# Optimization experiments

Hardware: AMD Instinct MI355X
Metric: run time of the kernel (lower is better)

The kernel has to match this reference:

```python
import jax, jax.numpy as jnp
import numpy as np

N = 40000      # total nodes in the batched graph
E = 640000     # total edges (avg degree 16)
F_IN = 1280    # num_features (ESM embedding dim)
H = 128        # hidden_dim
G = 64         # number of graphs in the batch
OUT = 273      # output_dim (GO terms)
NEG_SLOPE = 0.2
BN_EPS = 1e-5


def setup_inputs() -> dict:
    key = jax.random.key(0)
    ks = jax.random.split(key, 16)
    def nrm(k, shape, s=0.05):
        return jax.random.normal(k, shape, dtype=jnp.float32) * s
    inp = {}
    inp["x"] = jax.random.normal(ks[0], (N, F_IN), dtype=jnp.float32)
    inp["edge_index"] = jax.random.randint(ks[1], (2, E), 0, N, dtype=jnp.int32)
    inp["batch"] = jnp.sort(jax.random.randint(ks[2], (N,), 0, G, dtype=jnp.int32))
    inp["W1"] = nrm(ks[3], (F_IN, H)); inp["b1"] = jnp.zeros((H,), jnp.float32)
    inp["a_src1"] = nrm(ks[4], (H,)); inp["a_dst1"] = nrm(ks[5], (H,))
    inp["W2"] = nrm(ks[6], (H, H)); inp["b2"] = jnp.zeros((H,), jnp.float32)
    inp["a_src2"] = nrm(ks[7], (H,)); inp["a_dst2"] = nrm(ks[8], (H,))
    inp["W3"] = nrm(ks[9], (H, H)); inp["b3"] = jnp.zeros((H,), jnp.float32)
    inp["a_src3"] = nrm(ks[10], (H,)); inp["a_dst3"] = nrm(ks[11], (H,))
    inp["fc1_W"] = nrm(ks[12], (H, 1024)); inp["fc1_b"] = jnp.zeros((1024,), jnp.float32)
    inp["bn_g"] = jnp.ones((1024,), jnp.float32); inp["bn_b"] = jnp.zeros((1024,), jnp.float32)
    inp["bn_rm"] = jnp.zeros((1024,), jnp.float32); inp["bn_rv"] = jnp.ones((1024,), jnp.float32)
    inp["fc2_W"] = nrm(ks[13], (1024, OUT)); inp["fc2_b"] = jnp.zeros((OUT,), jnp.float32)
    return inp


def gat_layer(x, W, b, a_src, a_dst, src, dst, n_nodes):
    # single-head GAT ('gat_originated'): h = xW, e_ij = lrelu(a_src.h_j + a_dst.h_i)
    h = x @ W                                            # [N, H]
    e = jax.nn.leaky_relu((h @ a_src)[src] + (h @ a_dst)[dst], NEG_SLOPE)  # [E]
    # numerically-stable segment softmax over incoming edges of each target node
    m = jax.ops.segment_max(e, dst, num_segments=n_nodes)
    p = jnp.exp(e - m[dst])
    denom = jax.ops.segment_sum(p, dst, num_segments=n_nodes)
    alpha = p / (denom[dst] + 1e-16)                     # [E]
    out = jax.ops.segment_sum(alpha[:, None] * h[src], dst, num_segments=n_nodes)
    return out + b


def reference(x, edge_index, batch, W1, b1, a_src1, a_dst1, W2, b2, a_src2, a_dst2,
              W3, b3, a_src3, a_dst3, fc1_W, fc1_b, bn_g, bn_b, bn_rm, bn_rv, fc2_W, fc2_b):
    n = x.shape[0]
    src, dst = edge_index[0], edge_index[1]
    h = jax.nn.relu(gat_layer(x, W1, b1, a_src1, a_dst1, src, dst, n))
    h = jax.nn.relu(gat_layer(h, W2, b2, a_src2, a_dst2, src, dst, n))
    h = gat_layer(h, W3, b3, a_src3, a_dst3, src, dst, n)
    # gap: global mean pool per graph
    cnt = jax.ops.segment_sum(jnp.ones((n,), h.dtype), batch, num_segments=G)
    pooled = jax.ops.segment_sum(h, batch, num_segments=G) / jnp.maximum(cnt, 1.0)[:, None]
    z = pooled @ fc1_W + fc1_b                            # [G, 1024]
    z = (z - bn_rm) * jax.lax.rsqrt(bn_rv + BN_EPS) * bn_g + bn_b  # BN eval mode
    z = jax.nn.relu(z)                                    # dropout is identity in eval
    return jax.nn.sigmoid(z @ fc2_W + fc2_b)              # [G, 273]
```

## Files before the change

### kernel.cpp

```cpp
#include <hip/hip_runtime.h>
#include <math.h>

#define N_NODES 40000
#define N_EDGES 640000
#define F_IN    1280
#define H       128
#define NG      64
#define OUTD    273
#define FC1D    1024
#define NEG_SLOPE 0.2f
#define BN_EPS  1e-5f

typedef __attribute__((ext_vector_type(8))) short short8;
typedef __attribute__((ext_vector_type(4))) float f32x4;

__device__ __forceinline__ unsigned short f2bf(float f) {
    unsigned u = __float_as_uint(f);
    u += 0x7FFF + ((u >> 16) & 1);
    return (unsigned short)(u >> 16);
}
__device__ __forceinline__ float bf2f(unsigned short s) {
    return __uint_as_float((unsigned)s << 16);
}

__global__ void edge_hist(const int* __restrict__ dst, int* __restrict__ cnt, int e) {
    int i = blockIdx.x * blockDim.x + threadIdx.x;
    if (i < e) atomicAdd(&cnt[dst[i]], 1);
}

__global__ void scan_excl(const int* __restrict__ cnt, int* __restrict__ row_ptr, int n) {
    const int CH = 40;
    __shared__ int sm[1024];
    int tid = threadIdx.x;
    int start = tid * CH;
    int local[CH];
    int s = 0;
    #pragma unroll
    for (int k = 0; k < CH; ++k) {
        int i = start + k;
        int v = (i < n) ? cnt[i] : 0;
        local[k] = s;
        s += v;
    }
    sm[tid] = s;
    __syncthreads();
    for (int off = 1; off < 1024; off <<= 1) {
        int t = (tid >= off) ? sm[tid - off] : 0;
        __syncthreads();
        sm[tid] += t;
        __syncthreads();
    }
    int base = sm[tid] - s;
    #pragma unroll
    for (int k = 0; k < CH; ++k) {
        int i = start + k;
        if (i < n) row_ptr[i] = base + local[k];
    }
    if (tid == 1023) row_ptr[n] = sm[1023];
}

__global__ void edge_fill(const int* __restrict__ src, const int* __restrict__ dst,
                          const int* __restrict__ row_ptr, int* __restrict__ fill,
                          int* __restrict__ csr_src, int e) {
    int i = blockIdx.x * blockDim.x + threadIdx.x;
    if (i < e) {
        int d = dst[i];
        int pos = row_ptr[d] + atomicAdd(&fill[d], 1);
        csr_src[pos] = src[i];
    }
}

__global__ void wprep(const float* __restrict__ W, unsigned short* __restrict__ Bp, int K) {
    int i = blockIdx.x * blockDim.x + threadIdx.x;
    if (i >= K * H) return;
    int k = i >> 7, col = i & 127;
    float v = W[i];
    unsigned short hh = f2bf(v);
    unsigned short ll = f2bf(v - bf2f(hh));
    int t = k >> 6, rr = k & 63;
    int s = rr >> 5, r5 = rr & 31;
    int laneHi = r5 >> 3, j = r5 & 7;
    int lane = laneHi * 16 + (col & 15);
    int n = col >> 4;
    int U = (n * 2 + s) * 64 + lane;
    size_t idx = (size_t)t * 16384 + (size_t)U * 8 + j;
    Bp[idx] = hh;
    Bp[idx + 8192] = ll;
}

__device__ __forceinline__ void cvt8(float4 x, float4 y, short8& hi, short8& lo) {
    float f[8] = {x.x, x.y, x.z, x.w, y.x, y.y, y.z, y.w};
    #pragma unroll
    for (int j = 0; j < 8; ++j) {
        unsigned u = __float_as_uint(f[j]);
        unsigned short hh = (unsigned short)((u + 0x7FFF + ((u >> 16) & 1)) >> 16);
        hi[j] = (short)hh;
        float r = f[j] - __uint_as_float((unsigned)hh << 16);
        unsigned ur = __float_as_uint(r);
        lo[j] = (short)((ur + 0x7FFF + ((ur >> 16) & 1)) >> 16);
    }
}

__global__ __launch_bounds__(256) void gemm_fused(
    const float* __restrict__ A, const unsigned short* __restrict__ Bp,
    const float* __restrict__ a_src, const float* __restrict__ a_dst,
    unsigned short* __restrict__ hWb, float* __restrict__ hs,
    float* __restrict__ hd, int K)
{
    __shared__ __align__(16) unsigned short lds[16384];
    const int tid  = threadIdx.x;
    const int lane = tid & 63, wv = tid >> 6;
    const int fr = lane & 15, q = lane >> 4;
    const int m0 = blockIdx.x * 64;
    const int row = m0 + wv * 16 + fr;
    const int nt = K >> 6;

    const uint4* gb = (const uint4*)Bp + tid;
    uint4* lp = (uint4*)lds + tid;

    uint4 f0 = gb[0],    f1 = gb[256],  f2 = gb[512],  f3 = gb[768],
          f4 = gb[1024], f5 = gb[1280], f6 = gb[1536], f7 = gb[1792];

    f32x4 acc0 = {}, acc1 = {}, acc2 = {}, acc3 = {},
          acc4 = {}, acc5 = {}, acc6 = {}, acc7 = {};

    for (int t = 0; t < nt; ++t) {
        lp[0] = f0;    lp[256] = f1;  lp[512] = f2;  lp[768] = f3;
        lp[1024] = f4; lp[1280] = f5; lp[1536] = f6; lp[1792] = f7;
        if (t + 1 < nt) {
            const uint4* g = gb + (size_t)(t + 1) * 2048;
            f0 = g[0];    f1 = g[256];  f2 = g[512];  f3 = g[768];
            f4 = g[1024]; f5 = g[1280]; f6 = g[1536]; f7 = g[1792];
        }
        __syncthreads();

        const float* ap = A + (size_t)row * K + t * 64 + q * 8;
        float4 a0 = *(const float4*)(ap);
        float4 a1 = *(const float4*)(ap + 4);
        float4 a2 = *(const float4*)(ap + 32);
        float4 a3 = *(const float4*)(ap + 36);

        short8 ah, al;
#define MSTEP(nn, accv, ss)                                                     \
        {                                                                       \
            const short8 bh = *(const short8*)&lds[(size_t)(((nn)*2+(ss))*64 + lane)*8];          \
            const short8 bl = *(const short8*)&lds[(size_t)(((nn)*2+(ss))*64 + lane)*8 + 8192];   \
            accv = __builtin_amdgcn_mfma_f32_16x16x32_bf16(ah, bh, accv, 0, 0, 0);                \
            accv = __builtin_amdgcn_mfma_f32_16x16x32_bf16(ah, bl, accv, 0, 0, 0);                \
            accv = __builtin_amdgcn_mfma_f32_16x16x32_bf16(al, bh, accv, 0, 0, 0);                \
        }
        cvt8(a0, a1, ah, al);
        MSTEP(0, acc0, 0) MSTEP(1, acc1, 0) MSTEP(2, acc2, 0) MSTEP(3, acc3, 0)
        MSTEP(4, acc4, 0) MSTEP(5, acc5, 0) MSTEP(6, acc6, 0) MSTEP(7, acc7, 0)
        cvt8(a2, a3, ah, al);
        MSTEP(0, acc0, 1) MSTEP(1, acc1, 1) MSTEP(2, acc2, 1) MSTEP(3, acc3, 1)
        MSTEP(4, acc4, 1) MSTEP(5, acc5, 1) MSTEP(6, acc6, 1) MSTEP(7, acc7, 1)
#undef MSTEP
        __syncthreads();
    }

    const int rb = m0 + wv * 16 + q * 4;
#define EPI(nn, accv)                                                           \
    {                                                                           \
        _Pragma("unroll")                                                       \
        for (int i = 0; i < 4; ++i)                                             \
            hWb[(size_t)(rb + i) * H + (nn)*16 + fr] = f2bf(accv[i]);           \
    }
    EPI(0, acc0) EPI(1, acc1) EPI(2, acc2) EPI(3, acc3)
    EPI(4, acc4) EPI(5, acc5) EPI(6, acc6) EPI(7, acc7)
#undef EPI

    float asv[8], adv[8];
    #pragma unroll
    for (int n = 0; n < 8; ++n) {
        asv[n] = a_src[n * 16 + fr];
        adv[n] = a_dst[n * 16 + fr];
    }
    #pragma unroll
    for (int i = 0; i < 4; ++i) {
        float ss = acc0[i]*asv[0] + acc1[i]*asv[1] + acc2[i]*asv[2] + acc3[i]*asv[3]
                 + acc4[i]*asv[4] + acc5[i]*asv[5] + acc6[i]*asv[6] + acc7[i]*asv[7];
        float dd = acc0[i]*adv[0] + acc1[i]*adv[1] + acc2[i]*adv[2] + acc3[i]*adv[3]
                 + acc4[i]*adv[4] + acc5[i]*adv[5] + acc6[i]*adv[6] + acc7[i]*adv[7];
        #pragma unroll
        for (int off = 8; off; off >>= 1) {
            ss += __shfl_xor(ss, off);
            dd += __shfl_xor(dd, off);
        }
        if (fr == 0) { hs[rb + i] = ss; hd[rb + i] = dd; }
    }
}

__device__ __forceinline__ float bfhi(unsigned u) { return __uint_as_float(u << 16); }
__device__ __forceinline__ float bflo(unsigned u) { return __uint_as_float(u & 0xffff0000u); }

__global__ void attn_agg(const unsigned short* __restrict__ hWb,
                         const float* __restrict__ hs, const float* __restrict__ hd,
                         const int* __restrict__ row_ptr, const int* __restrict__ csr_src,
                         const float* __restrict__ bias, float* __restrict__ out,
                         int n, int relu_flag) {
    int wv = (blockIdx.x * blockDim.x + threadIdx.x) >> 6;
    int lane = threadIdx.x & 63;
    if (wv >= n) return;
    int p0 = row_ptr[wv], p1 = row_ptr[wv + 1];
    int deg = p1 - p0;
    float hdi = hd[wv];
    float ax = 0.f, ay = 0.f;
    const unsigned* hb = (const unsigned*)hWb;

    if (deg <= 64) {
        int valid = (lane < deg);
        int sidx = valid ? csr_src[p0 + lane] : 0;
        float e = hs[sidx] + hdi;
        e = (e >= 0.f) ? e : NEG_SLOPE * e;
        float ev = valid ? e : -3.4e38f;
        float m = ev;
        #pragma unroll
        for (int off = 32; off; off >>= 1) m = fmaxf(m, __shfl_xor(m, off));
        float pe = valid ? __expf(e - m) : 0.f;
        float dsum = pe;
        #pragma unroll
        for (int off = 32; off; off >>= 1) dsum += __shfl_xor(dsum, off);
        pe *= 1.f / (dsum + 1e-16f);

        int j = 0;
        int dq = deg & ~3;
        for (; j < dq; j += 4) {
            float al0 = __shfl(pe, j),     al1 = __shfl(pe, j + 1);
            float al2 = __shfl(pe, j + 2), al3 = __shfl(pe, j + 3);
            int s0 = __shfl(sidx, j),     s1 = __shfl(sidx, j + 1);
            int s2 = __shfl(sidx, j + 2), s3 = __shfl(sidx, j + 3);
            unsigned u0 = hb[(size_t)s0 * 64 + lane];
            unsigned u1 = hb[(size_t)s1 * 64 + lane];
            unsigned u2 = hb[(size_t)s2 * 64 + lane];
            unsigned u3 = hb[(size_t)s3 * 64 + lane];
            ax += al0 * bfhi(u0); ay += al0 * bflo(u0);
            ax += al1 * bfhi(u1); ay += al1 * bflo(u1);
            ax += al2 * bfhi(u2); ay += al2 * bflo(u2);
            ax += al3 * bfhi(u3); ay += al3 * bflo(u3);
        }
        for (; j < deg; ++j) {
            float alpha = __shfl(pe, j);
            int s = __shfl(sidx, j);
            unsigned u = hb[(size_t)s * 64 + lane];
            ax += alpha * bfhi(u); ay += alpha * bflo(u);
        }
    } else {
        float m = -3.4e38f;
        for (int p = p0 + lane; p < p1; p += 64) {
            float e = hs[csr_src[p]] + hdi;
            e = (e >= 0.f) ? e : NEG_SLOPE * e;
            m = fmaxf(m, e);
        }
        #pragma unroll
        for (int off = 32; off; off >>= 1) m = fmaxf(m, __shfl_xor(m, off));
        float dsum = 0.f;
        for (int p = p0 + lane; p < p1; p += 64) {
            float e = hs[csr_src[p]] + hdi;
            e = (e >= 0.f) ? e : NEG_SLOPE * e;
            dsum += __expf(e - m);
        }
        #pragma unroll
        for (int off = 32; off; off >>= 1) dsum += __shfl_xor(dsum, off);
        float inv = 1.f / (dsum + 1e-16f);
        for (int p = p0; p < p1; ++p) {
            int s = csr_src[p];
            float e = hs[s] + hdi;
            e = (e >= 0.f) ? e : NEG_SLOPE * e;
            float alpha = __expf(e - m) * inv;
            unsigned u = hb[(size_t)s * 64 + lane];
            ax += alpha * bfhi(u); ay += alpha * bflo(u);
        }
    }
    float2 bv = *(const float2*)&bias[2 * lane];
    float o0 = ax + bv.x;
    float o1 = ay + bv.y;
    if (relu_flag) { o0 = fmaxf(o0, 0.f); o1 = fmaxf(o1, 0.f); }
    float2 ov; ov.x = o0; ov.y = o1;
    *(float2*)&out[(size_t)wv * H + 2 * lane] = ov;
}

__device__ __forceinline__ void graph_range(const int* __restrict__ batch, int n,
                                            int g, int& start, int& end) {
    int lo = 0, hi = n;
    while (lo < hi) { int mid = (lo + hi) >> 1; if (batch[mid] < g) lo = mid + 1; else hi = mid; }
    start = lo;
    lo = start; hi = n;
    while (lo < hi) { int mid = (lo + hi) >> 1; if (batch[mid] < g + 1) lo = mid + 1; else hi = mid; }
    end = lo;
}

__global__ void pool_part(const float* __restrict__ h, const int* __restrict__ batch,
                          float* __restrict__ part, int n) {
    int g = blockIdx.x >> 3, c = blockIdx.x & 7;
    int f = threadIdx.x;
    int start, end;
    graph_range(batch, n, g, start, end);
    int len = end - start;
    int cs = start + (len * c) / 8, ce = start + (len * (c + 1)) / 8;
    float acc = 0.f;
    for (int i = cs; i < ce; ++i) acc += h[(size_t)i * H + f];
    part[((size_t)g * 8 + c) * H + f] = acc;
}

__global__ void pool_final(const float* __restrict__ part, const int* __restrict__ batch,
                           float* __restrict__ pooled, int n) {
    int g = blockIdx.x;
    int f = threadIdx.x;
    int start, end;
    graph_range(batch, n, g, start, end);
    float s = 0.f;
    #pragma unroll
    for (int c = 0; c < 8; ++c) s += part[((size_t)g * 8 + c) * H + f];
    float cnt = (float)(end - start);
    pooled[g * H + f] = s / fmaxf(cnt, 1.f);
}

__global__ void fc1_bn_relu(const float* __restrict__ pooled, const float* __restrict__ W,
                            const float* __restrict__ b, const float* __restrict__ bng,
                            const float* __restrict__ bnb, const float* __restrict__ bnrm,
                            const float* __restrict__ bnrv, float* __restrict__ z) {
    int g = blockIdx.x >> 2;
    int j = ((blockIdx.x & 3) << 8) + threadIdx.x;
    const float* pr = pooled + g * H;
    float acc = b[j];
    #pragma unroll 8
    for (int k = 0; k < H; ++k) acc += pr[k] * W[k * FC1D + j];
    float v = (acc - bnrm[j]) * rsqrtf(bnrv[j] + BN_EPS) * bng[j] + bnb[j];
    z[g * FC1D + j] = fmaxf(v, 0.f);
}

__global__ void fc2_sig(const float* __restrict__ z, const float* __restrict__ W,
                        const float* __restrict__ b, float* __restrict__ out) {
    int g = blockIdx.x;
    int j = threadIdx.x;
    if (j >= OUTD) return;
    const float* zr = z + g * FC1D;
    float acc = b[j];
    #pragma unroll 4
    for (int k = 0; k < FC1D; ++k) acc += zr[k] * W[k * OUTD + j];
    out[g * OUTD + j] = 1.f / (1.f + __expf(-acc));
}

extern "C" void kernel_launch(void* const* d_in, const int* in_sizes, int n_in,
                              void* d_out, int out_size, void* d_ws, size_t ws_size,
                              hipStream_t stream) {
    const float* x     = (const float*)d_in[0];
    const int*   eidx  = (const int*)d_in[1];
    const int*   batch = (const int*)d_in[2];
    const float* W1 = (const float*)d_in[3];  const float* b1 = (const float*)d_in[4];
    const float* as1 = (const float*)d_in[5]; const float* ad1 = (const float*)d_in[6];
    const float* W2 = (const float*)d_in[7];  const float* b2 = (const float*)d_in[8];
    const float* as2 = (const float*)d_in[9]; const float* ad2 = (const float*)d_in[10];
    const float* W3 = (const float*)d_in[11]; const float* b3 = (const float*)d_in[12];
    const float* as3 = (const float*)d_in[13]; const float* ad3 = (const float*)d_in[14];
    const float* fc1W = (const float*)d_in[15]; const float* fc1b = (const float*)d_in[16];
    const float* bng = (const float*)d_in[17];  const float* bnb = (const float*)d_in[18];
    const float* bnrm = (const float*)d_in[19]; const float* bnrv = (const float*)d_in[20];
    const float* fc2W = (const float*)d_in[21]; const float* fc2b = (const float*)d_in[22];
    const int* src = eidx;
    const int* dst = eidx + N_EDGES;

    float* hA      = (float*)d_ws;
    float* hs      = hA + (size_t)N_NODES * H;
    float* hd      = hs + N_NODES;
    float* pooled  = hd + N_NODES;
    float* part    = pooled + NG * H;
    float* z       = part + NG * 8 * H;
    unsigned short* hWb = (unsigned short*)(z + NG * FC1D);
    unsigned short* Bp1 = hWb + (size_t)N_NODES * H;
    unsigned short* Bp2 = Bp1 + (size_t)(F_IN / 64) * 16384;
    unsigned short* Bp3 = Bp2 + (size_t)(H / 64) * 16384;
    int*   row_ptr = (int*)(Bp3 + (size_t)(H / 64) * 16384);
    int*   row_cnt = row_ptr + (N_NODES + 1);
    int*   csr_src = row_cnt + N_NODES;

    const int EB = (N_EDGES + 255) / 256;
    const int NW = (N_NODES * 64 + 255) / 256;
    const int GB = N_NODES / 64;

    wprep<<<(F_IN * H + 255) / 256, 256, 0, stream>>>(W1, Bp1, F_IN);
    wprep<<<(H * H + 255) / 256, 256, 0, stream>>>(W2, Bp2, H);
    wprep<<<(H * H + 255) / 256, 256, 0, stream>>>(W3, Bp3, H);

    hipMemsetAsync(row_cnt, 0, N_NODES * sizeof(int), stream);
    edge_hist<<<EB, 256, 0, stream>>>(dst, row_cnt, N_EDGES);
    scan_excl<<<1, 1024, 0, stream>>>(row_cnt, row_ptr, N_NODES);
    hipMemsetAsync(row_cnt, 0, N_NODES * sizeof(int), stream);
    edge_fill<<<EB, 256, 0, stream>>>(src, dst, row_ptr, row_cnt, csr_src, N_EDGES);

    gemm_fused<<<GB, 256, 0, stream>>>(x, Bp1, as1, ad1, hWb, hs, hd, F_IN);
    attn_agg<<<NW, 256, 0, stream>>>(hWb, hs, hd, row_ptr, csr_src, b1, hA, N_NODES, 1);
    gemm_fused<<<GB, 256, 0, stream>>>(hA, Bp2, as2, ad2, hWb, hs, hd, H);
    attn_agg<<<NW, 256, 0, stream>>>(hWb, hs, hd, row_ptr, csr_src, b2, hA, N_NODES, 1);
    gemm_fused<<<GB, 256, 0, stream>>>(hA, Bp3, as3, ad3, hWb, hs, hd, H);
    attn_agg<<<NW, 256, 0, stream>>>(hWb, hs, hd, row_ptr, csr_src, b3, hA, N_NODES, 0);

    pool_part<<<NG * 8, H, 0, stream>>>(hA, batch, part, N_NODES);
    pool_final<<<NG, H, 0, stream>>>(part, batch, pooled, N_NODES);
    fc1_bn_relu<<<NG * 4, 256, 0, stream>>>(pooled, fc1W, fc1b, bng, bnb, bnrm, bnrv, z);
    fc2_sig<<<NG, 320, 0, stream>>>(z, fc2W, fc2b, (float*)d_out);
}
```

Baseline: 744.9 us.

## Double-buffer GEMM LDS tiles, prefetch neighbor rows in attention, merge weight prep

The fused GEMM now uses two LDS buffers and software-prefetches both B tiles and A fragments one step ahead, with the loop unrolled by two, so global loads overlap the MFMA work. The attention aggregation issues loads for the first 16 neighbor feature rows before the softmax reduction, hiding gather latency behind the max/sum shuffles. The three weight-prep launches are merged into one kernel to cut launch overhead. The cost is doubled LDS and more registers, which may lower occupancy. The unroll-by-two loop assumes an even tile count, which holds for K=1280 and K=128.

Measured after the change: 742.8 us. Within noise of the previous version (-0.3%).

```diff
diff --git a/kernel.cpp b/kernel.cpp
--- a/kernel.cpp
+++ b/kernel.cpp
@@ -70,9 +70,9 @@
     }
 }
 
-__global__ void wprep(const float* __restrict__ W, unsigned short* __restrict__ Bp, int K) {
-    int i = blockIdx.x * blockDim.x + threadIdx.x;
-    if (i >= K * H) return;
+__device__ __forceinline__ void wprep_one(const float* __restrict__ W,
+                                          unsigned short* __restrict__ Bp,
+                                          int i, int K) {
     int k = i >> 7, col = i & 127;
     float v = W[i];
     unsigned short hh = f2bf(v);
@@ -88,6 +88,18 @@
     Bp[idx + 8192] = ll;
 }
 
+__global__ void wprep_all(const float* __restrict__ W1, const float* __restrict__ W2,
+                          const float* __restrict__ W3, unsigned short* __restrict__ Bp1,
+                          unsigned short* __restrict__ Bp2, unsigned short* __restrict__ Bp3) {
+    int i = blockIdx.x * blockDim.x + threadIdx.x;
+    const int n1 = F_IN * H, n2 = H * H;
+    if (i < n1) { wprep_one(W1, Bp1, i, F_IN); return; }
+    i -= n1;
+    if (i < n2) { wprep_one(W2, Bp2, i, H); return; }
+    i -= n2;
+    if (i < n2) { wprep_one(W3, Bp3, i, H); }
+}
+
 __device__ __forceinline__ void cvt8(float4 x, float4 y, short8& hi, short8& lo) {
     float f[8] = {x.x, x.y, x.z, x.w, y.x, y.y, y.z, y.w};
     #pragma unroll
@@ -107,7 +119,7 @@
     unsigned short* __restrict__ hWb, float* __restrict__ hs,
     float* __restrict__ hd, int K)
 {
-    __shared__ __align__(16) unsigned short lds[16384];
+    __shared__ __align__(16) unsigned short lds[2][16384];
     const int tid  = threadIdx.x;
     const int lane = tid & 63, wv = tid >> 6;
     const int fr = lane & 15, q = lane >> 4;
@@ -116,48 +128,67 @@
     const int nt = K >> 6;
 
     const uint4* gb = (const uint4*)Bp + tid;
-    uint4* lp = (uint4*)lds + tid;
-
-    uint4 f0 = gb[0],    f1 = gb[256],  f2 = gb[512],  f3 = gb[768],
-          f4 = gb[1024], f5 = gb[1280], f6 = gb[1536], f7 = gb[1792];
+    const float* Aptr = A + (size_t)row * K + q * 8;
 
     f32x4 acc0 = {}, acc1 = {}, acc2 = {}, acc3 = {},
           acc4 = {}, acc5 = {}, acc6 = {}, acc7 = {};
 
-    for (int t = 0; t < nt; ++t) {
-        lp[0] = f0;    lp[256] = f1;  lp[512] = f2;  lp[768] = f3;
-        lp[1024] = f4; lp[1280] = f5; lp[1536] = f6; lp[1792] = f7;
-        if (t + 1 < nt) {
-            const uint4* g = gb + (size_t)(t + 1) * 2048;
-            f0 = g[0];    f1 = g[256];  f2 = g[512];  f3 = g[768];
-            f4 = g[1024]; f5 = g[1280]; f6 = g[1536]; f7 = g[1792];
-        }
+    uint4 bA0, bA1, bA2, bA3, bA4, bA5, bA6, bA7;
+    uint4 bB0, bB1, bB2, bB3, bB4, bB5, bB6, bB7;
+    float4 aA0, aA1, aA2, aA3, aB0, aB1, aB2, aB3;
+
+#define LOADB(t, r0, r1, r2, r3, r4, r5, r6, r7)                                \
+    { const uint4* g = gb + (size_t)(t) * 2048;                                 \
+      r0 = g[0];    r1 = g[256];  r2 = g[512];  r3 = g[768];                    \
+      r4 = g[1024]; r5 = g[1280]; r6 = g[1536]; r7 = g[1792]; }
+#define LOADA(t, x0, x1, x2, x3)                                                \
+    { const float* ap = Aptr + (size_t)(t) * 64;                                \
+      x0 = *(const float4*)(ap);      x1 = *(const float4*)(ap + 4);            \
+      x2 = *(const float4*)(ap + 32); x3 = *(const float4*)(ap + 36); }
+#define STAGE(buf, r0, r1, r2, r3, r4, r5, r6, r7)                              \
+    { uint4* lp = (uint4*)lds[buf] + tid;                                       \
+      lp[0] = r0;    lp[256] = r1;  lp[512] = r2;  lp[768] = r3;                \
+      lp[1024] = r4; lp[1280] = r5; lp[1536] = r6; lp[1792] = r7; }
+#define MSTEP(buf, nn, accv, ss)                                                \
+    { const short8 bh = *(const short8*)&lds[buf][(size_t)(((nn)*2+(ss))*64 + lane)*8];        \
+      const short8 bl = *(const short8*)&lds[buf][(size_t)(((nn)*2+(ss))*64 + lane)*8 + 8192]; \
+      accv = __builtin_amdgcn_mfma_f32_16x16x32_bf16(ah, bh, accv, 0, 0, 0);    \
+      accv = __builtin_amdgcn_mfma_f32_16x16x32_bf16(ah, bl, accv, 0, 0, 0);    \
+      accv = __builtin_amdgcn_mfma_f32_16x16x32_bf16(al, bh, accv, 0, 0, 0); }
+#define COMPUTE(buf, x0, x1, x2, x3)                                            \
+    { short8 ah, al;                                                            \
+      cvt8(x0, x1, ah, al);                                                     \
+      MSTEP(buf, 0, acc0, 0) MSTEP(buf, 1, acc1, 0) MSTEP(buf, 2, acc2, 0)      \
+      MSTEP(buf, 3, acc3, 0) MSTEP(buf, 4, acc4, 0) MSTEP(buf, 5, acc5, 0)      \
+      MSTEP(buf, 6, acc6, 0) MSTEP(buf, 7, acc7, 0)                             \
+      cvt8(x2, x3, ah, al);                                                     \
+      MSTEP(buf, 0, acc0, 1) MSTEP(buf, 1, acc1, 1) MSTEP(buf, 2, acc2, 1)      \
+      MSTEP(buf, 3, acc3, 1) MSTEP(buf, 4, acc4, 1) MSTEP(buf, 5, acc5, 1)      \
+      MSTEP(buf, 6, acc6, 1) MSTEP(buf, 7, acc7, 1) }
+
+    LOADB(0, bA0, bA1, bA2, bA3, bA4, bA5, bA6, bA7);
+    LOADA(0, aA0, aA1, aA2, aA3);
+
+    for (int t = 0; t < nt; t += 2) {
+        STAGE(0, bA0, bA1, bA2, bA3, bA4, bA5, bA6, bA7);
+        LOADB(t + 1, bB0, bB1, bB2, bB3, bB4, bB5, bB6, bB7);
+        LOADA(t + 1, aB0, aB1, aB2, aB3);
         __syncthreads();
-
-        const float* ap = A + (size_t)row * K + t * 64 + q * 8;
-        float4 a0 = *(const float4*)(ap);
-        float4 a1 = *(const float4*)(ap + 4);
-        float4 a2 = *(const float4*)(ap + 32);
-        float4 a3 = *(const float4*)(ap + 36);
-
-        short8 ah, al;
-#define MSTEP(nn, accv, ss)                                                     \
-        {                                                                       \
-            const short8 bh = *(const short8*)&lds[(size_t)(((nn)*2+(ss))*64 + lane)*8];          \
-            const short8 bl = *(const short8*)&lds[(size_t)(((nn)*2+(ss))*64 + lane)*8 + 8192];   \
-            accv = __builtin_amdgcn_mfma_f32_16x16x32_bf16(ah, bh, accv, 0, 0, 0);                \
-            accv = __builtin_amdgcn_mfma_f32_16x16x32_bf16(ah, bl, accv, 0, 0, 0);                \
-            accv = __builtin_amdgcn_mfma_f32_16x16x32_bf16(al, bh, accv, 0, 0, 0);                \
-        }
-        cvt8(a0, a1, ah, al);
-        MSTEP(0, acc0, 0) MSTEP(1, acc1, 0) MSTEP(2, acc2, 0) MSTEP(3, acc3, 0)
-        MSTEP(4, acc4, 0) MSTEP(5, acc5, 0) MSTEP(6, acc6, 0) MSTEP(7, acc7, 0)
-        cvt8(a2, a3, ah, al);
-        MSTEP(0, acc0, 1) MSTEP(1, acc1, 1) MSTEP(2, acc2, 1) MSTEP(3, acc3, 1)
-        MSTEP(4, acc4, 1) MSTEP(5, acc5, 1) MSTEP(6, acc6, 1) MSTEP(7, acc7, 1)
+        COMPUTE(0, aA0, aA1, aA2, aA3);
+
+        STAGE(1, bB0, bB1, bB2, bB3, bB4, bB5, bB6, bB7);
+        if (t + 2 < nt) {
+            LOADB(t + 2, bA0, bA1, bA2, bA3, bA4, bA5, bA6, bA7);
+            LOADA(t + 2, aA0, aA1, aA2, aA3);
+        }
+        __syncthreads();
+        COMPUTE(1, aB0, aB1, aB2, aB3);
+    }
+#undef LOADB
+#undef LOADA
+#undef STAGE
 #undef MSTEP
-        __syncthreads();
-    }
+#undef COMPUTE
 
     const int rb = m0 + wv * 16 + q * 4;
 #define EPI(nn, accv)                                                           \
@@ -211,10 +242,16 @@
     if (deg <= 64) {
         int valid = (lane < deg);
         int sidx = valid ? csr_src[p0 + lane] : 0;
+
+#define PF(k) int s_##k = __shfl(sidx, k); unsigned u_##k = 0;                  \
+              if (deg > k) u_##k = hb[(size_t)s_##k * 64 + lane];
+        PF(0)  PF(1)  PF(2)  PF(3)  PF(4)  PF(5)  PF(6)  PF(7)
+        PF(8)  PF(9)  PF(10) PF(11) PF(12) PF(13) PF(14) PF(15)
+#undef PF
+
         float e = hs[sidx] + hdi;
         e = (e >= 0.f) ? e : NEG_SLOPE * e;
-        float ev = valid ? e : -3.4e38f;
-        float m = ev;
+        float m = valid ? e : -3.4e38f;
         #pragma unroll
         for (int off = 32; off; off >>= 1) m = fmaxf(m, __shfl_xor(m, off));
         float pe = valid ? __expf(e - m) : 0.f;
@@ -223,27 +260,29 @@
         for (int off = 32; off; off >>= 1) dsum += __shfl_xor(dsum, off);
         pe *= 1.f / (dsum + 1e-16f);
 
-        int j = 0;
-        int dq = deg & ~3;
-        for (; j < dq; j += 4) {
-            float al0 = __shfl(pe, j),     al1 = __shfl(pe, j + 1);
-            float al2 = __shfl(pe, j + 2), al3 = __shfl(pe, j + 3);
-            int s0 = __shfl(sidx, j),     s1 = __shfl(sidx, j + 1);
-            int s2 = __shfl(sidx, j + 2), s3 = __shfl(sidx, j + 3);
-            unsigned u0 = hb[(size_t)s0 * 64 + lane];
-            unsigned u1 = hb[(size_t)s1 * 64 + lane];
-            unsigned u2 = hb[(size_t)s2 * 64 + lane];
-            unsigned u3 = hb[(size_t)s3 * 64 + lane];
-            ax += al0 * bfhi(u0); ay += al0 * bflo(u0);
-            ax += al1 * bfhi(u1); ay += al1 * bflo(u1);
-            ax += al2 * bfhi(u2); ay += al2 * bflo(u2);
-            ax += al3 * bfhi(u3); ay += al3 * bflo(u3);
-        }
-        for (; j < deg; ++j) {
-            float alpha = __shfl(pe, j);
-            int s = __shfl(sidx, j);
-            unsigned u = hb[(size_t)s * 64 + lane];
-            ax += alpha * bfhi(u); ay += alpha * bflo(u);
+#define AC(k) if (deg > k) { float aa = __shfl(pe, k);                          \
+                             ax += aa * bfhi(u_##k); ay += aa * bflo(u_##k); }
+        AC(0)  AC(1)  AC(2)  AC(3)  AC(4)  AC(5)  AC(6)  AC(7)
+        AC(8)  AC(9)  AC(10) AC(11) AC(12) AC(13) AC(14) AC(15)
+#undef AC
+
+        for (int j = 16; j < deg; j += 4) {
+            int t0 = __shfl(sidx, j);
+            int t1 = (j + 1 < deg) ? __shfl(sidx, j + 1) : t0;
+            int t2 = (j + 2 < deg) ? __shfl(sidx, j + 2) : t0;
+            int t3 = (j + 3 < deg) ? __shfl(sidx, j + 3) : t0;
+            unsigned v0 = hb[(size_t)t0 * 64 + lane];
+            unsigned v1 = hb[(size_t)t1 * 64 + lane];
+            unsigned v2 = hb[(size_t)t2 * 64 + lane];
+            unsigned v3 = hb[(size_t)t3 * 64 + lane];
+            float b0 = __shfl(pe, j);
+            float b1 = (j + 1 < deg) ? __shfl(pe, j + 1) : 0.f;
+            float b2 = (j + 2 < deg) ? __shfl(pe, j + 2) : 0.f;
+            float b3 = (j + 3 < deg) ? __shfl(pe, j + 3) : 0.f;
+            ax += b0 * bfhi(v0); ay += b0 * bflo(v0);
+            ax += b1 * bfhi(v1); ay += b1 * bflo(v1);
+            ax += b2 * bfhi(v2); ay += b2 * bflo(v2);
+            ax += b3 * bfhi(v3); ay += b3 * bflo(v3);
         }
     } else {
         float m = -3.4e38f;
@@ -379,9 +418,8 @@
     const int NW = (N_NODES * 64 + 255) / 256;
     const int GB = N_NODES / 64;
 
-    wprep<<<(F_IN * H + 255) / 256, 256, 0, stream>>>(W1, Bp1, F_IN);
-    wprep<<<(H * H + 255) / 256, 256, 0, stream>>>(W2, Bp2, H);
-    wprep<<<(H * H + 255) / 256, 256, 0, stream>>>(W3, Bp3, H);
+    const int WTOT = F_IN * H + 2 * H * H;
+    wprep_all<<<(WTOT + 255) / 256, 256, 0, stream>>>(W1, W2, W3, Bp1, Bp2, Bp3);
 
     hipMemsetAsync(row_cnt, 0, N_NODES * sizeof(int), stream);
     edge_hist<<<EB, 256, 0, stream>>>(dst, row_cnt, N_EDGES);
```
